# Kernel tuning notes

Hardware: AMD Instinct MI355X
Metric: run time of the kernel (lower is better)

## Reference

```python
import jax, jax.numpy as jnp
import numpy as np
import math

B, C, W = 4, 256, 64
GROUPS = 32
EPS = 1e-6


def setup_inputs() -> dict:
    key = jax.random.key(0)
    ks = jax.random.split(key, 6)
    xavier = math.sqrt(2.0 / (C + C))
    return {
        "x": jax.random.normal(ks[0], (B, C, W, W), dtype=jnp.float32),
        "gn_gamma": jnp.ones((C,), dtype=jnp.float32),
        "gn_beta": jnp.zeros((C,), dtype=jnp.float32),
        "wq": jax.random.normal(ks[1], (C, C), dtype=jnp.float32) * xavier,
        "bq": jnp.zeros((C,), dtype=jnp.float32),
        "wk": jax.random.normal(ks[2], (C, C), dtype=jnp.float32) * xavier,
        "bk": jnp.zeros((C,), dtype=jnp.float32),
        "wv": jax.random.normal(ks[3], (C, C), dtype=jnp.float32) * xavier,
        "bv": jnp.zeros((C,), dtype=jnp.float32),
        "wo": jax.random.normal(ks[4], (C, C), dtype=jnp.float32) * 1e-5,
        "bo": jnp.zeros((C,), dtype=jnp.float32),
    }


def _nin(w, b, t):
    # 1x1 conv via shared weights: [O,C] x [B,C,H,W] -> [B,O,H,W]
    return jnp.einsum('oc,bchw->bohw', w, t) + b[None, :, None, None]


def _group_norm(x, gamma, beta):
    b, c, h, w = x.shape
    xr = x.reshape(b, GROUPS, c // GROUPS, h, w)
    mu = xr.mean(axis=(2, 3, 4), keepdims=True)
    var = xr.var(axis=(2, 3, 4), keepdims=True)
    xn = ((xr - mu) / jnp.sqrt(var + EPS)).reshape(b, c, h, w)
    return xn * gamma[None, :, None, None] + beta[None, :, None, None]


def reference(x, gn_gamma, gn_beta, wq, bq, wk, bk, wv, bv, wo, bo):
    b, c, wdt, _ = x.shape
    n = wdt * wdt  # number of spatial tokens
    h = _group_norm(x, gn_gamma, gn_beta)
    q = _nin(wq, bq, h).reshape(b, c, n)
    k = _nin(wk, bk, h).reshape(b, c, n)
    v = _nin(wv, bv, h).reshape(b, c, n)
    scale = 1.0 / math.sqrt(c)
    scores = jnp.einsum('bcn,bcm->bnm', q, k) * scale  # [B, N, N]
    attn = jax.nn.softmax(scores, axis=-1)
    o = jnp.einsum('bnm,bcm->bcn', attn, v).reshape(b, c, wdt, wdt)
    return x + _nin(wo, bo, o)
```

## Files before the change

### kernel.cpp

```cpp
#include <hip/hip_runtime.h>
#include <math.h>

#define B_      4
#define C_      256
#define NTOK    4096
#define GROUPS_ 32
#define CPG_    8
#define EPS_    1e-6f
#define QSCALE  (0.0625f * 1.4426950408889634f)
#define NSEG    4
#define KSEG    (NTOK / NSEG)
#define QB      128

typedef __attribute__((ext_vector_type(8)))  short short8v;
typedef __attribute__((ext_vector_type(4)))  float float4v;
typedef __attribute__((ext_vector_type(16))) float f32x16;
typedef __attribute__((ext_vector_type(4)))  unsigned short ushort4v;
typedef unsigned short ushort_t;

__device__ __forceinline__ ushort_t f2bf(float f) {
  union { float f; unsigned u; } v; v.f = f;
  unsigned r = (v.u + 0x7FFFu + ((v.u >> 16) & 1u)) >> 16;
  return (ushort_t)r;
}
__device__ __forceinline__ float bf2f(ushort_t u) {
  union { unsigned u; float f; } v; v.u = ((unsigned)u) << 16; return v.f;
}
__device__ __forceinline__ unsigned cvtpk(float lo, float hi) {
  unsigned r;
  asm("v_cvt_pk_bf16_f32 %0, %1, %2" : "=v"(r) : "v"(lo), "v"(hi));
  return r;
}
__device__ __forceinline__ float exp2_hw(float x) {
  float r;
  asm("v_exp_f32 %0, %1" : "=v"(r) : "v"(x));
  return r;
}

__device__ __forceinline__ float4v mfma16(short8v a, short8v b, float4v c) {
  return __builtin_amdgcn_mfma_f32_16x16x32_bf16(a, b, c, 0, 0, 0);
}
__device__ __forceinline__ f32x16 mfma32(short8v a, short8v b, f32x16 c) {
  return __builtin_amdgcn_mfma_f32_32x32x16_bf16(a, b, c, 0, 0, 0);
}

__device__ __forceinline__ void gld16(const ushort_t* g, ushort_t* l) {
  __builtin_amdgcn_global_load_lds(
      (const __attribute__((address_space(1))) unsigned int*)g,
      (__attribute__((address_space(3))) unsigned int*)l, 16, 0, 0);
}

__global__ __launch_bounds__(256) void prep(
    const float* __restrict__ x,
    const float* __restrict__ wq, const float* __restrict__ wk,
    const float* __restrict__ wv, const float* __restrict__ wo,
    float* __restrict__ stats, ushort_t* __restrict__ Wb) {
  const int t = threadIdx.x;
  if (blockIdx.x < 128) {
    const int bg = blockIdx.x;
    const size_t base = (size_t)bg * CPG_ * NTOK;
    float s = 0.f, s2 = 0.f;
    for (int i = t * 4; i < CPG_ * NTOK; i += 1024) {
      float4 v = *reinterpret_cast<const float4*>(x + base + i);
      s  += v.x + v.y + v.z + v.w;
      s2 += v.x * v.x + v.y * v.y + v.z * v.z + v.w * v.w;
    }
    #pragma unroll
    for (int m = 32; m >= 1; m >>= 1) { s += __shfl_xor(s, m); s2 += __shfl_xor(s2, m); }
    __shared__ float red[8];
    const int wv_ = t >> 6;
    if ((t & 63) == 0) { red[wv_] = s; red[4 + wv_] = s2; }
    __syncthreads();
    if (t == 0) {
      float ts  = red[0] + red[1] + red[2] + red[3];
      float ts2 = red[4] + red[5] + red[6] + red[7];
      const float inv_n = 1.0f / (float)(CPG_ * NTOK);
      float mu  = ts * inv_n;
      float var = ts2 * inv_n - mu * mu;
      stats[bg * 2]     = mu;
      stats[bg * 2 + 1] = rsqrtf(var + EPS_);
    }
  } else {
    const int id = blockIdx.x - 128;
    const int m = id >> 6;
    const float* srcs[4] = {wq, wk, wv, wo};
    const float* s = srcs[m];
    const int i = ((id & 63) * 256 + t) * 4;
    float4 v = *reinterpret_cast<const float4*>(s + i);
    ushort4v o4 = {f2bf(v.x), f2bf(v.y), f2bf(v.z), f2bf(v.w)};
    *reinterpret_cast<ushort4v*>(Wb + (size_t)m * 65536 + i) = o4;
  }
}

__global__ __launch_bounds__(256) void qkv_gn(
    const ushort_t* __restrict__ Wb, const float* __restrict__ bq,
    const float* __restrict__ bk, const float* __restrict__ bv,
    const float* __restrict__ x, const float* __restrict__ stats,
    const float* __restrict__ gamma, const float* __restrict__ beta,
    ushort_t* __restrict__ Qt, ushort_t* __restrict__ Kt,
    ushort_t* __restrict__ Vv) {
  const int b  = blockIdx.y;
  const int n0 = blockIdx.x * 32;
  const int t  = threadIdx.x;
  const int w  = t >> 6, l = t & 63;
  const int lg = l >> 4, ln = l & 15;
  __shared__ __align__(16) ushort_t Hs[32][264];
  const float* xb = x + (size_t)b * C_ * NTOK;
  #pragma unroll
  for (int j = 0; j < 8; ++j) {
    const int f4 = t + 256 * j;
    const int c  = f4 >> 3;
    const int nq = (f4 & 7) * 4;
    float4 v = *reinterpret_cast<const float4*>(xb + (size_t)c * NTOK + n0 + nq);
    const float mu = stats[(b * GROUPS_ + (c >> 3)) * 2];
    const float rs = stats[(b * GROUPS_ + (c >> 3)) * 2 + 1];
    const float ga = gamma[c] * rs;
    const float be = beta[c] - mu * ga;
    Hs[nq + 0][c] = f2bf(v.x * ga + be);
    Hs[nq + 1][c] = f2bf(v.y * ga + be);
    Hs[nq + 2][c] = f2bf(v.z * ga + be);
    Hs[nq + 3][c] = f2bf(v.w * ga + be);
  }
  __syncthreads();

  auto gemm = [&](const ushort_t* W, float4v acc[4][2]) {
    #pragma unroll
    for (int mt = 0; mt < 4; ++mt)
      #pragma unroll
      for (int nt = 0; nt < 2; ++nt) acc[mt][nt] = (float4v){0.f, 0.f, 0.f, 0.f};
    const ushort_t* Wrow = W + (size_t)(64 * w + ln) * C_;
    #pragma unroll
    for (int kk = 0; kk < 8; ++kk) {
      short8v af[4], bfr[2];
      #pragma unroll
      for (int mt = 0; mt < 4; ++mt)
        af[mt] = *reinterpret_cast<const short8v*>(Wrow + mt * 16 * C_ + kk * 32 + 8 * lg);
      #pragma unroll
      for (int nt = 0; nt < 2; ++nt)
        bfr[nt] = *reinterpret_cast<const short8v*>(&Hs[nt * 16 + ln][kk * 32 + 8 * lg]);
      #pragma unroll
      for (int mt = 0; mt < 4; ++mt)
        #pragma unroll
        for (int nt = 0; nt < 2; ++nt)
          acc[mt][nt] = mfma16(af[mt], bfr[nt], acc[mt][nt]);
    }
  };

  float4v acc[4][2];
  #pragma unroll
  for (int m = 0; m < 2; ++m) {
    const float* bias = (m == 0) ? bq : bk;
    const float osc = (m == 0) ? QSCALE : 1.0f;
    ushort_t* dst = (m == 0) ? Qt : Kt;
    gemm(Wb + (size_t)m * 65536, acc);
    #pragma unroll
    for (int mt = 0; mt < 4; ++mt) {
      const int mb = 64 * w + mt * 16 + 4 * lg;
      #pragma unroll
      for (int nt = 0; nt < 2; ++nt) {
        const int n = n0 + nt * 16 + ln;
        ushort4v pk;
        #pragma unroll
        for (int r = 0; r < 4; ++r)
          pk[r] = f2bf((acc[mt][nt][r] + bias[mb + r]) * osc);
        *reinterpret_cast<ushort4v*>(dst + ((size_t)b * NTOK + n) * C_ + mb) = pk;
      }
    }
  }
  gemm(Wb + 2 * 65536, acc);
  #pragma unroll
  for (int mt = 0; mt < 4; ++mt) {
    const int mb = 64 * w + mt * 16 + 4 * lg;
    #pragma unroll
    for (int nt = 0; nt < 2; ++nt) {
      const int n = n0 + nt * 16 + ln;
      const int k  = n & 31, kb = n >> 5;
      const int e  = (k & 3) | (((k >> 3) & 1) << 2);
      const int o  = ((k >> 2) & 1) | (((k >> 4) & 1) << 1);
      #pragma unroll
      for (int r = 0; r < 4; ++r) {
        const int c = mb + r;
        const int s = o ^ ((c >> 1) & 3);
        Vv[((size_t)b * (NTOK / 32) + kb) * (C_ * 32) + (size_t)c * 32 + s * 8 + e] =
            f2bf(acc[mt][nt][r] + bv[mb + r]);
      }
    }
  }
}

__global__ __launch_bounds__(256, 2) void flash14(
    const ushort_t* __restrict__ Qt, const ushort_t* __restrict__ Kt,
    const ushort_t* __restrict__ Vg, ushort_t* __restrict__ O0,
    ushort_t* __restrict__ Orest, float2* __restrict__ ml) {
  const int id  = blockIdx.x;
  const int xcd = id & 7, sq = id >> 3;
  const int combo = xcd + 8 * (sq >> 5);
  const int b   = combo & 3;
  const int seg = combo >> 2;
  const int q0  = (sq & 31) * QB;
  const int t = threadIdx.x, w = t >> 6, l = t & 63;
  const int ln = l & 31, hi = l >> 5;

  __shared__ __align__(16) ushort_t Ks[2][32][256];
  __shared__ __align__(16) ushort_t Vs[2][8192];

  const ushort_t* Kb_ = Kt + (size_t)b * NTOK * C_;
  const ushort_t* Vb_ = Vg + (size_t)b * NTOK * C_;

  short8v qf[16];
  {
    const ushort_t* qrow = Qt + ((size_t)b * NTOK + q0 + 32 * w + ln) * C_ + 8 * hi;
    #pragma unroll
    for (int kk = 0; kk < 16; ++kk)
      qf[kk] = *reinterpret_cast<const short8v*>(qrow + 16 * kk);
  }

  f32x16 Oacc[8];
  #pragma unroll
  for (int ct = 0; ct < 8; ++ct)
    #pragma unroll
    for (int r = 0; r < 16; ++r) Oacc[ct][r] = 0.f;
  float m_run = -1e30f, l_run = 0.f;

  const int kbase = seg * KSEG;
  const int NT = KSEG / 32;

  auto STAGE_K = [&](int buf, int k0) {
    #pragma unroll
    for (int j = 0; j < 4; ++j) {
      const int i   = 4 * w + j;
      const int row = 2 * i + (l >> 5);
      const int nn  = (l & 31) ^ (row & 15);
      gld16(Kb_ + (size_t)(k0 + row) * C_ + 8 * nn, &Ks[buf][2 * i][0]);
    }
  };
  auto STAGE_V = [&](int buf, int k0) {
    const ushort_t* vt = Vb_ + (size_t)(k0 >> 5) * (C_ * 32);
    #pragma unroll
    for (int j = 0; j < 4; ++j) {
      const int i = 4 * w + j;
      gld16(vt + i * 512 + 8 * l, &Vs[buf][i * 512]);
    }
  };

  int cur = 0;
  STAGE_K(0, kbase);
  STAGE_V(0, kbase);

  for (int it = 0; it < NT; ++it) {
    asm volatile("s_waitcnt vmcnt(4)" ::: "memory");
    __builtin_amdgcn_sched_barrier(0);
    __syncthreads();
    const bool pre = (it + 1 < NT);
    if (pre) {
      const int nxt = kbase + 32 * (it + 1);
      STAGE_K(cur ^ 1, nxt);
      STAGE_V(cur ^ 1, nxt);
    }

    f32x16 sA, sB;
    #pragma unroll
    for (int r = 0; r < 16; ++r) { sA[r] = 0.f; sB[r] = 0.f; }
    const ushort_t* Kc = &Ks[cur][0][0];
    __builtin_amdgcn_s_setprio(1);
    #pragma unroll
    for (int kk = 0; kk < 16; kk += 2) {
      short8v k0f = *reinterpret_cast<const short8v*>(
          Kc + ln * 256 + 8 * ((2 * kk + hi) ^ (ln & 15)));
      short8v k1f = *reinterpret_cast<const short8v*>(
          Kc + ln * 256 + 8 * ((2 * kk + 2 + hi) ^ (ln & 15)));
      sA = mfma32(k0f, qf[kk], sA);
      sB = mfma32(k1f, qf[kk + 1], sB);
    }
    __builtin_amdgcn_s_setprio(0);
    f32x16 sacc = sA + sB;

    float mx8[8];
    #pragma unroll
    for (int j = 0; j < 8; ++j) mx8[j] = fmaxf(sacc[j], sacc[j + 8]);
    #pragma unroll
    for (int j = 0; j < 4; ++j) mx8[j] = fmaxf(mx8[j], mx8[j + 4]);
    float pmax = fmaxf(fmaxf(mx8[0], mx8[2]), fmaxf(mx8[1], mx8[3]));
    pmax = fmaxf(pmax, __shfl_xor(pmax, 32));
    if (!__all(pmax - m_run <= 11.0f)) {
      const float mnew = fmaxf(m_run, pmax);
      const float alpha = exp2_hw(m_run - mnew);
      m_run = mnew;
      l_run *= alpha;
      float av[16];
      #pragma unroll
      for (int r = 0; r < 16; ++r)
        av[r] = __shfl(alpha, (r & 3) + 8 * (r >> 2) + 4 * hi);
      #pragma unroll
      for (int ct = 0; ct < 8; ++ct)
        #pragma unroll
        for (int r = 0; r < 16; ++r) Oacc[ct][r] *= av[r];
    }
    float sm8[8];
    #pragma unroll
    for (int r = 0; r < 16; ++r) sacc[r] = exp2_hw(sacc[r] - m_run);
    #pragma unroll
    for (int j = 0; j < 8; ++j) sm8[j] = sacc[j] + sacc[j + 8];
    #pragma unroll
    for (int j = 0; j < 4; ++j) sm8[j] += sm8[j + 4];
    float ps = (sm8[0] + sm8[2]) + (sm8[1] + sm8[3]);
    ps += __shfl_xor(ps, 32);
    l_run += ps;

    union { unsigned u[4]; short8v v; } P0, P1;
    #pragma unroll
    for (int j = 0; j < 4; ++j) {
      P0.u[j] = cvtpk(sacc[2 * j], sacc[2 * j + 1]);
      P1.u[j] = cvtpk(sacc[8 + 2 * j], sacc[9 + 2 * j]);
    }
    const short8v pa0 = P0.v, pa1 = P1.v;

    if (pre) asm volatile("s_waitcnt vmcnt(8)" ::: "memory");
    else     asm volatile("s_waitcnt vmcnt(0)" ::: "memory");
    __builtin_amdgcn_sched_barrier(0);
    __syncthreads();

    const ushort_t* Vc = &Vs[cur][0];
    const int sx = (ln >> 1) & 3;
    __builtin_amdgcn_s_setprio(1);
    #pragma unroll
    for (int ct = 0; ct < 8; ++ct) {
      const int c = 32 * ct + ln;
      const ushort_t* vr = Vc + c * 32;
      short8v v0 = *reinterpret_cast<const short8v*>(vr + 8 * (hi ^ sx));
      short8v v1 = *reinterpret_cast<const short8v*>(vr + 8 * ((2 | hi) ^ sx));
      Oacc[ct] = mfma32(pa0, v0, Oacc[ct]);
      Oacc[ct] = mfma32(pa1, v1, Oacc[ct]);
    }
    __builtin_amdgcn_s_setprio(0);
    cur ^= 1;
  }

  ushort_t* Op = (seg == 0 ? O0 : Orest + (size_t)(seg - 1) * (size_t)B_ * NTOK * C_)
               + (size_t)b * NTOK * C_;
  #pragma unroll
  for (int ct = 0; ct < 8; ++ct)
    #pragma unroll
    for (int r = 0; r < 16; ++r) {
      const int qr = q0 + 32 * w + (r & 3) + 8 * (r >> 2) + 4 * hi;
      Op[(size_t)qr * C_ + 32 * ct + ln] = f2bf(Oacc[ct][r]);
    }
  if (hi == 0)
    ml[(seg * B_ + b) * NTOK + q0 + 32 * w + ln] = make_float2(m_run, l_run);
}

__global__ __launch_bounds__(256) void nin_final(
    const ushort_t* __restrict__ Wo, const float* __restrict__ bo,
    const ushort_t* __restrict__ O0, const ushort_t* __restrict__ Orest,
    const float2* __restrict__ ml, const float* __restrict__ xres,
    float* __restrict__ out) {
  const int b  = blockIdx.y;
  const int n0 = blockIdx.x * 32;
  const int t  = threadIdx.x;
  const int w  = t >> 6, l = t & 63;
  const int lg = l >> 4, ln = l & 15;
  __shared__ __align__(16) ushort_t Hs[32][264];
  const size_t SLOT = (size_t)B_ * NTOK * C_;
  #pragma unroll
  for (int it = 0; it < 4; ++it) {
    const int idx = t + 256 * it;
    const int row = idx >> 5;
    const int ch  = (idx & 31) * 8;
    const int n   = n0 + row;
    float m4[NSEG], l4[NSEG], M = -1e30f;
    #pragma unroll
    for (int s = 0; s < NSEG; ++s) {
      float2 v = ml[(s * B_ + b) * NTOK + n];
      m4[s] = v.x; l4[s] = v.y;
      M = fmaxf(M, v.x);
    }
    float L = 0.f, wsc[NSEG];
    #pragma unroll
    for (int s = 0; s < NSEG; ++s) { wsc[s] = exp2_hw(m4[s] - M); L += wsc[s] * l4[s]; }
    const float inv = 1.0f / L;
    float acc8[8];
    #pragma unroll
    for (int j = 0; j < 8; ++j) acc8[j] = 0.f;
    #pragma unroll
    for (int s = 0; s < NSEG; ++s) {
      const ushort_t* op = (s == 0 ? O0 : Orest + (size_t)(s - 1) * SLOT);
      short8v v = *reinterpret_cast<const short8v*>(
          op + ((size_t)b * NTOK + n) * C_ + ch);
      #pragma unroll
      for (int j = 0; j < 8; ++j) acc8[j] += wsc[s] * bf2f((ushort_t)v[j]);
    }
    union { ushort_t us[8]; short8v v; } o8;
    #pragma unroll
    for (int j = 0; j < 8; ++j) o8.us[j] = f2bf(acc8[j] * inv);
    *reinterpret_cast<short8v*>(&Hs[row][ch]) = o8.v;
  }
  __syncthreads();

  float4v acc[4][2];
  #pragma unroll
  for (int mt = 0; mt < 4; ++mt)
    #pragma unroll
    for (int nt = 0; nt < 2; ++nt) acc[mt][nt] = (float4v){0.f, 0.f, 0.f, 0.f};
  const ushort_t* Wrow = Wo + (size_t)(64 * w + ln) * C_;
  #pragma unroll
  for (int kk = 0; kk < 8; ++kk) {
    short8v af[4], bfr[2];
    #pragma unroll
    for (int mt = 0; mt < 4; ++mt)
      af[mt] = *reinterpret_cast<const short8v*>(Wrow + mt * 16 * C_ + kk * 32 + 8 * lg);
    #pragma unroll
    for (int nt = 0; nt < 2; ++nt)
      bfr[nt] = *reinterpret_cast<const short8v*>(&Hs[nt * 16 + ln][kk * 32 + 8 * lg]);
    #pragma unroll
    for (int mt = 0; mt < 4; ++mt)
      #pragma unroll
      for (int nt = 0; nt < 2; ++nt)
        acc[mt][nt] = mfma16(af[mt], bfr[nt], acc[mt][nt]);
  }
  #pragma unroll
  for (int mt = 0; mt < 4; ++mt) {
    const int mb = 64 * w + mt * 16 + 4 * lg;
    #pragma unroll
    for (int nt = 0; nt < 2; ++nt) {
      const int n = n0 + nt * 16 + ln;
      #pragma unroll
      for (int r = 0; r < 4; ++r) {
        const size_t off = ((size_t)b * C_ + mb + r) * NTOK + n;
        out[off] = acc[mt][nt][r] + bo[mb + r] + xres[off];
      }
    }
  }
}

extern "C" void kernel_launch(void* const* d_in, const int* in_sizes, int n_in,
                              void* d_out, int out_size, void* d_ws, size_t ws_size,
                              hipStream_t stream) {
  (void)in_sizes; (void)n_in; (void)out_size; (void)ws_size;
  const float* x     = (const float*)d_in[0];
  const float* gamma = (const float*)d_in[1];
  const float* beta  = (const float*)d_in[2];
  const float* wq    = (const float*)d_in[3];
  const float* bq    = (const float*)d_in[4];
  const float* wk    = (const float*)d_in[5];
  const float* bk    = (const float*)d_in[6];
  const float* wv    = (const float*)d_in[7];
  const float* bv    = (const float*)d_in[8];
  const float* wo    = (const float*)d_in[9];
  const float* bo    = (const float*)d_in[10];
  float* out = (float*)d_out;

  ushort_t* ws16 = (ushort_t*)d_ws;
  const size_t SLOT = (size_t)B_ * NTOK * C_;

  ushort_t* Op0 = ws16;
  ushort_t* Qt  = ws16 + SLOT;
  ushort_t* Kt  = ws16 + 2 * SLOT;
  ushort_t* Vb  = ws16 + 3 * SLOT;
  ushort_t* OpR = ws16 + 4 * SLOT;
  ushort_t* Wb  = ws16 + 7 * SLOT;
  float*  stats = (float*)(Wb + 4 * 65536);
  float2* mlp   = (float2*)(stats + 256);

  prep<<<dim3(384), 256, 0, stream>>>(x, wq, wk, wv, wo, stats, Wb);

  dim3 gg(NTOK / 32, B_);
  qkv_gn<<<gg, 256, 0, stream>>>(Wb, bq, bk, bv, x, stats, gamma, beta,
                                 Qt, Kt, Vb);

  flash14<<<dim3(NSEG * B_ * (NTOK / QB)), 256, 0, stream>>>(Qt, Kt, Vb, Op0, OpR, mlp);

  nin_final<<<gg, 256, 0, stream>>>(Wb + 3 * 65536, bo, Op0, OpR, mlp, x, out);
}
```

Before: 157.3 us.

## Switch flash attention to 16x16 MFMA tiles with 64-query blocks

The flash kernel moves from 32x32x16 to 16x16x32 bf16 MFMA. Each wave now handles 16 queries instead of 32, the query block shrinks from 128 to 64, and the grid doubles. The V tile becomes single-buffered, which frees LDS and registers so occupancy can go from 2 to 3 blocks per CU, and the V layout written by qkv_gn changes to match the new fragment order. The trade is twice the K/V reloads per query and shallower prefetch of V, in exchange for more resident waves and smaller per-wave state.

```diff
diff --git a/kernel.cpp b/kernel.cpp
--- a/kernel.cpp
+++ b/kernel.cpp
@@ -10,11 +10,10 @@
 #define QSCALE  (0.0625f * 1.4426950408889634f)
 #define NSEG    4
 #define KSEG    (NTOK / NSEG)
-#define QB      128
+#define QB      64
 
 typedef __attribute__((ext_vector_type(8)))  short short8v;
 typedef __attribute__((ext_vector_type(4)))  float float4v;
-typedef __attribute__((ext_vector_type(16))) float f32x16;
 typedef __attribute__((ext_vector_type(4)))  unsigned short ushort4v;
 typedef unsigned short ushort_t;
 
@@ -39,9 +38,6 @@
 
 __device__ __forceinline__ float4v mfma16(short8v a, short8v b, float4v c) {
   return __builtin_amdgcn_mfma_f32_16x16x32_bf16(a, b, c, 0, 0, 0);
-}
-__device__ __forceinline__ f32x16 mfma32(short8v a, short8v b, f32x16 c) {
-  return __builtin_amdgcn_mfma_f32_32x32x16_bf16(a, b, c, 0, 0, 0);
 }
 
 __device__ __forceinline__ void gld16(const ushort_t* g, ushort_t* l) {
@@ -175,51 +171,48 @@
     for (int nt = 0; nt < 2; ++nt) {
       const int n = n0 + nt * 16 + ln;
       const int k  = n & 31, kb = n >> 5;
-      const int e  = (k & 3) | (((k >> 3) & 1) << 2);
-      const int o  = ((k >> 2) & 1) | (((k >> 4) & 1) << 1);
+      const int g  = (k >> 2) & 3;
+      const int jj = (k & 3) | (((k >> 4) & 1) << 2);
       #pragma unroll
       for (int r = 0; r < 4; ++r) {
         const int c = mb + r;
-        const int s = o ^ ((c >> 1) & 3);
-        Vv[((size_t)b * (NTOK / 32) + kb) * (C_ * 32) + (size_t)c * 32 + s * 8 + e] =
+        Vv[((size_t)b * (NTOK / 32) + kb) * (C_ * 32) + (size_t)c * 32 + g * 8 + jj] =
             f2bf(acc[mt][nt][r] + bv[mb + r]);
       }
     }
   }
 }
 
-__global__ __launch_bounds__(256, 2) void flash14(
+__global__ __launch_bounds__(256, 3) void flash15(
     const ushort_t* __restrict__ Qt, const ushort_t* __restrict__ Kt,
     const ushort_t* __restrict__ Vg, ushort_t* __restrict__ O0,
     ushort_t* __restrict__ Orest, float2* __restrict__ ml) {
   const int id  = blockIdx.x;
   const int xcd = id & 7, sq = id >> 3;
-  const int combo = xcd + 8 * (sq >> 5);
+  const int combo = xcd + 8 * (sq >> 6);
   const int b   = combo & 3;
   const int seg = combo >> 2;
-  const int q0  = (sq & 31) * QB;
+  const int q0  = (sq & 63) * QB;
   const int t = threadIdx.x, w = t >> 6, l = t & 63;
-  const int ln = l & 31, hi = l >> 5;
+  const int ln = l & 15, lg = l >> 4;
 
   __shared__ __align__(16) ushort_t Ks[2][32][256];
-  __shared__ __align__(16) ushort_t Vs[2][8192];
+  __shared__ __align__(16) ushort_t Vs[8192];
 
   const ushort_t* Kb_ = Kt + (size_t)b * NTOK * C_;
   const ushort_t* Vb_ = Vg + (size_t)b * NTOK * C_;
 
-  short8v qf[16];
+  short8v qf[8];
   {
-    const ushort_t* qrow = Qt + ((size_t)b * NTOK + q0 + 32 * w + ln) * C_ + 8 * hi;
-    #pragma unroll
-    for (int kk = 0; kk < 16; ++kk)
-      qf[kk] = *reinterpret_cast<const short8v*>(qrow + 16 * kk);
-  }
-
-  f32x16 Oacc[8];
-  #pragma unroll
-  for (int ct = 0; ct < 8; ++ct)
-    #pragma unroll
-    for (int r = 0; r < 16; ++r) Oacc[ct][r] = 0.f;
+    const ushort_t* qrow = Qt + ((size_t)b * NTOK + q0 + 16 * w + ln) * C_ + 8 * lg;
+    #pragma unroll
+    for (int kk = 0; kk < 8; ++kk)
+      qf[kk] = *reinterpret_cast<const short8v*>(qrow + 32 * kk);
+  }
+
+  float4v Oacc[16];
+  #pragma unroll
+  for (int ct = 0; ct < 16; ++ct) Oacc[ct] = (float4v){0.f, 0.f, 0.f, 0.f};
   float m_run = -1e30f, l_run = 0.f;
 
   const int kbase = seg * KSEG;
@@ -234,119 +227,100 @@
       gld16(Kb_ + (size_t)(k0 + row) * C_ + 8 * nn, &Ks[buf][2 * i][0]);
     }
   };
-  auto STAGE_V = [&](int buf, int k0) {
+  auto STAGE_V = [&](int k0) {
     const ushort_t* vt = Vb_ + (size_t)(k0 >> 5) * (C_ * 32);
     #pragma unroll
     for (int j = 0; j < 4; ++j) {
       const int i = 4 * w + j;
-      gld16(vt + i * 512 + 8 * l, &Vs[buf][i * 512]);
+      gld16(vt + i * 512 + 8 * l, &Vs[i * 512]);
     }
   };
 
-  int cur = 0;
   STAGE_K(0, kbase);
-  STAGE_V(0, kbase);
 
   for (int it = 0; it < NT; ++it) {
-    asm volatile("s_waitcnt vmcnt(4)" ::: "memory");
+    asm volatile("s_waitcnt vmcnt(0)" ::: "memory");
     __builtin_amdgcn_sched_barrier(0);
     __syncthreads();
     const bool pre = (it + 1 < NT);
-    if (pre) {
-      const int nxt = kbase + 32 * (it + 1);
-      STAGE_K(cur ^ 1, nxt);
-      STAGE_V(cur ^ 1, nxt);
-    }
-
-    f32x16 sA, sB;
-    #pragma unroll
-    for (int r = 0; r < 16; ++r) { sA[r] = 0.f; sB[r] = 0.f; }
-    const ushort_t* Kc = &Ks[cur][0][0];
+    STAGE_V(kbase + 32 * it);
+    if (pre) STAGE_K((it + 1) & 1, kbase + 32 * (it + 1));
+
+    float4v s0 = (float4v){0.f, 0.f, 0.f, 0.f};
+    float4v s1 = (float4v){0.f, 0.f, 0.f, 0.f};
+    const ushort_t* Kc = &Ks[it & 1][0][0];
     __builtin_amdgcn_s_setprio(1);
     #pragma unroll
-    for (int kk = 0; kk < 16; kk += 2) {
-      short8v k0f = *reinterpret_cast<const short8v*>(
-          Kc + ln * 256 + 8 * ((2 * kk + hi) ^ (ln & 15)));
-      short8v k1f = *reinterpret_cast<const short8v*>(
-          Kc + ln * 256 + 8 * ((2 * kk + 2 + hi) ^ (ln & 15)));
-      sA = mfma32(k0f, qf[kk], sA);
-      sB = mfma32(k1f, qf[kk + 1], sB);
+    for (int kk = 0; kk < 8; ++kk) {
+      const int ch = 8 * ((4 * kk + lg) ^ ln);
+      short8v kf0 = *reinterpret_cast<const short8v*>(Kc + ln * 256 + ch);
+      short8v kf1 = *reinterpret_cast<const short8v*>(Kc + (16 + ln) * 256 + ch);
+      s0 = mfma16(kf0, qf[kk], s0);
+      s1 = mfma16(kf1, qf[kk], s1);
     }
     __builtin_amdgcn_s_setprio(0);
-    f32x16 sacc = sA + sB;
-
-    float mx8[8];
-    #pragma unroll
-    for (int j = 0; j < 8; ++j) mx8[j] = fmaxf(sacc[j], sacc[j + 8]);
-    #pragma unroll
-    for (int j = 0; j < 4; ++j) mx8[j] = fmaxf(mx8[j], mx8[j + 4]);
-    float pmax = fmaxf(fmaxf(mx8[0], mx8[2]), fmaxf(mx8[1], mx8[3]));
+
+    float pmax = fmaxf(fmaxf(fmaxf(s0[0], s0[1]), fmaxf(s0[2], s0[3])),
+                       fmaxf(fmaxf(s1[0], s1[1]), fmaxf(s1[2], s1[3])));
+    pmax = fmaxf(pmax, __shfl_xor(pmax, 16));
     pmax = fmaxf(pmax, __shfl_xor(pmax, 32));
     if (!__all(pmax - m_run <= 11.0f)) {
       const float mnew = fmaxf(m_run, pmax);
       const float alpha = exp2_hw(m_run - mnew);
       m_run = mnew;
       l_run *= alpha;
-      float av[16];
-      #pragma unroll
-      for (int r = 0; r < 16; ++r)
-        av[r] = __shfl(alpha, (r & 3) + 8 * (r >> 2) + 4 * hi);
-      #pragma unroll
-      for (int ct = 0; ct < 8; ++ct)
+      float av[4];
+      #pragma unroll
+      for (int r = 0; r < 4; ++r) av[r] = __shfl(alpha, 4 * lg + r);
+      #pragma unroll
+      for (int ct = 0; ct < 16; ++ct)
         #pragma unroll
-        for (int r = 0; r < 16; ++r) Oacc[ct][r] *= av[r];
-    }
-    float sm8[8];
-    #pragma unroll
-    for (int r = 0; r < 16; ++r) sacc[r] = exp2_hw(sacc[r] - m_run);
-    #pragma unroll
-    for (int j = 0; j < 8; ++j) sm8[j] = sacc[j] + sacc[j + 8];
-    #pragma unroll
-    for (int j = 0; j < 4; ++j) sm8[j] += sm8[j + 4];
-    float ps = (sm8[0] + sm8[2]) + (sm8[1] + sm8[3]);
+        for (int r = 0; r < 4; ++r) Oacc[ct][r] *= av[r];
+    }
+    #pragma unroll
+    for (int r = 0; r < 4; ++r) {
+      s0[r] = exp2_hw(s0[r] - m_run);
+      s1[r] = exp2_hw(s1[r] - m_run);
+    }
+    float ps = (s0[0] + s0[1]) + (s0[2] + s0[3]) +
+               (s1[0] + s1[1]) + (s1[2] + s1[3]);
+    ps += __shfl_xor(ps, 16);
     ps += __shfl_xor(ps, 32);
     l_run += ps;
 
-    union { unsigned u[4]; short8v v; } P0, P1;
-    #pragma unroll
-    for (int j = 0; j < 4; ++j) {
-      P0.u[j] = cvtpk(sacc[2 * j], sacc[2 * j + 1]);
-      P1.u[j] = cvtpk(sacc[8 + 2 * j], sacc[9 + 2 * j]);
-    }
-    const short8v pa0 = P0.v, pa1 = P1.v;
-
-    if (pre) asm volatile("s_waitcnt vmcnt(8)" ::: "memory");
+    union { unsigned u[4]; short8v v; } P;
+    P.u[0] = cvtpk(s0[0], s0[1]);
+    P.u[1] = cvtpk(s0[2], s0[3]);
+    P.u[2] = cvtpk(s1[0], s1[1]);
+    P.u[3] = cvtpk(s1[2], s1[3]);
+    const short8v pa = P.v;
+
+    if (pre) asm volatile("s_waitcnt vmcnt(4)" ::: "memory");
     else     asm volatile("s_waitcnt vmcnt(0)" ::: "memory");
     __builtin_amdgcn_sched_barrier(0);
     __syncthreads();
 
-    const ushort_t* Vc = &Vs[cur][0];
-    const int sx = (ln >> 1) & 3;
     __builtin_amdgcn_s_setprio(1);
     #pragma unroll
-    for (int ct = 0; ct < 8; ++ct) {
-      const int c = 32 * ct + ln;
-      const ushort_t* vr = Vc + c * 32;
-      short8v v0 = *reinterpret_cast<const short8v*>(vr + 8 * (hi ^ sx));
-      short8v v1 = *reinterpret_cast<const short8v*>(vr + 8 * ((2 | hi) ^ sx));
-      Oacc[ct] = mfma32(pa0, v0, Oacc[ct]);
-      Oacc[ct] = mfma32(pa1, v1, Oacc[ct]);
+    for (int ct = 0; ct < 16; ++ct) {
+      const int c = 16 * ct + ln;
+      short8v vf = *reinterpret_cast<const short8v*>(Vs + c * 32 + 8 * lg);
+      Oacc[ct] = mfma16(pa, vf, Oacc[ct]);
     }
     __builtin_amdgcn_s_setprio(0);
-    cur ^= 1;
   }
 
   ushort_t* Op = (seg == 0 ? O0 : Orest + (size_t)(seg - 1) * (size_t)B_ * NTOK * C_)
                + (size_t)b * NTOK * C_;
   #pragma unroll
-  for (int ct = 0; ct < 8; ++ct)
-    #pragma unroll
-    for (int r = 0; r < 16; ++r) {
-      const int qr = q0 + 32 * w + (r & 3) + 8 * (r >> 2) + 4 * hi;
-      Op[(size_t)qr * C_ + 32 * ct + ln] = f2bf(Oacc[ct][r]);
-    }
-  if (hi == 0)
-    ml[(seg * B_ + b) * NTOK + q0 + 32 * w + ln] = make_float2(m_run, l_run);
+  for (int ct = 0; ct < 16; ++ct)
+    #pragma unroll
+    for (int r = 0; r < 4; ++r) {
+      const int qr = q0 + 16 * w + 4 * lg + r;
+      Op[(size_t)qr * C_ + 16 * ct + ln] = f2bf(Oacc[ct][r]);
+    }
+  if (l < 16)
+    ml[(seg * B_ + b) * NTOK + q0 + 16 * w + l] = make_float2(m_run, l_run);
 }
 
 __global__ __launch_bounds__(256) void nin_final(
@@ -467,7 +441,7 @@
   qkv_gn<<<gg, 256, 0, stream>>>(Wb, bq, bk, bv, x, stats, gamma, beta,
                                  Qt, Kt, Vb);
 
-  flash14<<<dim3(NSEG * B_ * (NTOK / QB)), 256, 0, stream>>>(Qt, Kt, Vb, Op0, OpR, mlp);
+  flash15<<<dim3(NSEG * B_ * (NTOK / QB)), 256, 0, stream>>>(Qt, Kt, Vb, Op0, OpR, mlp);
 
   nin_final<<<gg, 256, 0, stream>>>(Wb + 3 * 65536, bo, Op0, OpR, mlp, x, out);
 }
```

Result: slower. 175.5 us (+11.6%).
